# Performance work log

Hardware: AMD Instinct MI355X
Metric: run time of the kernel (lower is better)

Reference implementation:

```python
import jax, jax.numpy as jnp
import numpy as np

# static sizes
B, N_PER, D, H, L, DFF, IN_DIM = 32, 1024, 128, 4, 3, 2048, 64
N = B * N_PER
HD = D // H
EPS = 1e-5


def setup_inputs() -> dict:
    key = jax.random.key(0)
    ks = jax.random.split(key, 16)
    s = 0.02
    rn = lambda k, shp: jax.random.normal(k, shp, jnp.float32) * s
    return {
        "x": jax.random.normal(ks[0], (N, IN_DIM), jnp.float32),
        # uniform graph sizes -> static max_nodes; sorted graph ids
        "batch": jnp.repeat(jnp.arange(B, dtype=jnp.int32), N_PER),
        "W_in": rn(ks[1], (D, IN_DIM)),
        "b_in": rn(ks[2], (D,)),
        "Wqkv": rn(ks[3], (L, 3 * D, D)),
        "bqkv": rn(ks[4], (L, 3 * D)),
        "Wo": rn(ks[5], (L, D, D)),
        "bo": rn(ks[6], (L, D)),
        "W1": rn(ks[7], (L, DFF, D)),
        "b1": rn(ks[8], (L, DFF)),
        "W2": rn(ks[9], (L, D, DFF)),
        "b2": rn(ks[10], (L, D)),
        "ln1_g": jnp.ones((L, D), jnp.float32),
        "ln1_b": jnp.zeros((L, D), jnp.float32),
        "ln2_g": jnp.ones((L, D), jnp.float32),
        "ln2_b": jnp.zeros((L, D), jnp.float32),
    }


def _ln(x, g, b):
    m = x.mean(-1, keepdims=True)
    v = jnp.mean((x - m) ** 2, axis=-1, keepdims=True)
    return (x - m) / jnp.sqrt(v + EPS) * g + b


def _mha(h, Wqkv, bqkv, Wo, bo):
    # h: [B, S, D]
    qkv = h @ Wqkv.T + bqkv                      # [B, S, 3D]
    q, k, v = jnp.split(qkv, 3, axis=-1)
    q = q.reshape(B, -1, H, HD)
    k = k.reshape(B, -1, H, HD)
    v = v.reshape(B, -1, H, HD)
    att = jnp.einsum("bqhd,bkhd->bhqk", q, k) / np.sqrt(HD).astype(np.float32)
    p = jax.nn.softmax(att, axis=-1)
    o = jnp.einsum("bhqk,bkhd->bqhd", p, v).reshape(B, -1, D)
    return o @ Wo.T + bo


def reference(x, batch, W_in, b_in, Wqkv, bqkv, Wo, bo, W1, b1, W2, b2,
              ln1_g, ln1_b, ln2_g, ln2_b):
    # fused ragged -> padded: project all nodes once, scatter by (graph, pos)
    h = x @ W_in.T + b_in                        # [N, D]
    starts = jnp.searchsorted(batch, jnp.arange(B, dtype=batch.dtype))
    pos = jnp.arange(N, dtype=batch.dtype) - starts[batch]
    padded = jnp.zeros((B, N_PER, D), h.dtype).at[batch, pos].set(h)

    out = padded
    for l in range(L):  # post-LN TransformerEncoderLayer, dropout=eval
        a = _mha(out, Wqkv[l], bqkv[l], Wo[l], bo[l])
        out = _ln(out + a, ln1_g[l], ln1_b[l])
        f = jax.nn.relu(out @ W1[l].T + b1[l]) @ W2[l].T + b2[l]
        out = _ln(out + f, ln2_g[l], ln2_b[l])

    # mask derived from projected inputs, exactly as the original
    mask = (padded.sum(axis=2) != 0).astype(out.dtype)  # [B, S]
    return (out * mask[:, :, None]).sum(axis=1) / mask.sum(axis=1, keepdims=True)
```

## Files before the change

kernel.cpp:

```cpp
#include <hip/hip_runtime.h>
#include <hip/hip_bf16.h>
#include <stdint.h>

#define BB    32
#define NPER  1024
#define NTOT  32768
#define DD    128
#define HH    4
#define HD    32
#define LL    3
#define DFF   2048
#define INDIM 64
#define QKSCALE 0.17677669529663687f

typedef unsigned short u16;
typedef short bf16x8 __attribute__((ext_vector_type(8)));
typedef float f32x4 __attribute__((ext_vector_type(4)));

#define AS_GLOBAL(p) ((const __attribute__((address_space(1))) void*)(p))
#define AS_LDS(p)    ((__attribute__((address_space(3))) void*)(p))

__device__ __forceinline__ float bf2f(u16 v){
  unsigned u = ((unsigned)v) << 16; float f; __builtin_memcpy(&f, &u, 4); return f;
}
__device__ __forceinline__ u16 f2bf(float f){
  unsigned u; __builtin_memcpy(&u, &f, 4);
  unsigned lsb = (u >> 16) & 1u;
  u += 0x7fffu + lsb;
  return (u16)(u >> 16);
}

constexpr size_t OFF_FLAG   = 0;
constexpr size_t OFF_STARTS = 256;
constexpr size_t OFF_BIN    = 1024;
constexpr size_t OFF_BQKV   = OFF_BIN   + 128*4;
constexpr size_t OFF_BO     = OFF_BQKV  + 1152*4;
constexpr size_t OFF_B1     = OFF_BO    + 384*4;
constexpr size_t OFF_B2     = OFF_B1    + 6144*4;
constexpr size_t OFF_LN1G   = OFF_B2    + 384*4;
constexpr size_t OFF_LN1B   = OFF_LN1G  + 384*4;
constexpr size_t OFF_LN2G   = OFF_LN1B  + 384*4;
constexpr size_t OFF_LN2B   = OFF_LN2G  + 384*4;
constexpr size_t OFF_XB     = 40960;
constexpr size_t OFF_WINB   = OFF_XB    + (size_t)2097152*2;
constexpr size_t OFF_WQKVB  = OFF_WINB  + (size_t)8192*2;
constexpr size_t OFF_WOB    = OFF_WQKVB + (size_t)147456*2;
constexpr size_t OFF_W1B    = OFF_WOB   + (size_t)49152*2;
constexpr size_t OFF_W2B    = OFF_W1B   + (size_t)786432*2;
constexpr size_t OFF_CUR    = OFF_W2B   + (size_t)786432*2;
constexpr size_t OFF_TMP    = OFF_CUR   + (size_t)4194304*4;
constexpr size_t OFF_CURB   = OFF_TMP   + (size_t)4194304*4;
constexpr size_t OFF_QKVB   = OFF_CURB  + (size_t)4194304*2;
constexpr size_t OFF_ATTNOB = OFF_QKVB  + (size_t)12582912*2;
constexpr size_t OFF_ACTB   = OFF_ATTNOB+ (size_t)4194304*2;
constexpr size_t OFF_MASK   = OFF_ACTB  + (size_t)16777216*2;
constexpr size_t OFF_VT     = OFF_MASK  + (size_t)NTOT*4;
constexpr size_t OFF_RED    = OFF_VT    + (size_t)4096*1024*2;
constexpr size_t OFF_CNT    = OFF_RED   + (size_t)32*8*128*4;

__device__ __forceinline__ int plaus(unsigned bits){
  if ((bits << 1) == 0u) return 1;
  unsigned e = (bits >> 23) & 0xFFu;
  return (e >= 100u && e <= 140u) ? 1 : 0;
}
__global__ void detect_kernel(const unsigned* __restrict__ x, int* __restrict__ flag){
  __shared__ int red[256];
  int t = threadIdx.x, c = 0;
  for (int i = t; i < 2048; i += 256){
    unsigned w = x[i];
    c += (plaus(w << 16) & plaus(w & 0xFFFF0000u));
  }
  red[t] = c; __syncthreads();
  for (int s = 128; s > 0; s >>= 1){ if (t < s) red[t] += red[t+s]; __syncthreads(); }
  if (t == 0) *flag = (red[0] >= 1229) ? 1 : 0;
}

__global__ void starts_kernel(const int* __restrict__ batch, int* __restrict__ starts){
  int b = threadIdx.x;
  if (b < BB){
    int lo = 0, hi = NTOT;
    while (lo < hi){ int mid = (lo + hi) >> 1; if (batch[mid] < b) lo = mid + 1; else hi = mid; }
    starts[b] = lo;
  }
}

struct ConvSeg { const void* src; void* dst; int n; int tobf; };
struct ConvArgs { ConvSeg s[15]; };

__global__ __launch_bounds__(256) void convall_kernel(ConvArgs a, const int* __restrict__ flag){
  const int isb = *flag;
  const int blk = blockIdx.x;
  int seg = -1, base = 0, lb = 0;
  #pragma unroll
  for (int i = 0; i < 15; ++i){
    int nb = (a.s[i].n + 1023) >> 10;
    if (seg < 0){
      if (blk < base + nb){ seg = i; lb = blk - base; }
      base += nb;
    }
  }
  const ConvSeg sg = a.s[seg];
  const int idx = lb*1024 + threadIdx.x*4;
  if (idx >= sg.n) return;
  if (sg.tobf){
    u16* dst = (u16*)sg.dst + idx;
    if (isb){
      *(uint2*)dst = *(const uint2*)((const u16*)sg.src + idx);
    } else {
      const float* s4 = (const float*)sg.src + idx;
      dst[0] = f2bf(s4[0]); dst[1] = f2bf(s4[1]);
      dst[2] = f2bf(s4[2]); dst[3] = f2bf(s4[3]);
    }
  } else {
    float* dst = (float*)sg.dst + idx;
    if (isb){
      const u16* s4 = (const u16*)sg.src + idx;
      dst[0] = bf2f(s4[0]); dst[1] = bf2f(s4[1]);
      dst[2] = bf2f(s4[2]); dst[3] = bf2f(s4[3]);
    } else {
      *(float4*)dst = *(const float4*)((const float*)sg.src + idx);
    }
  }
}

__global__ __launch_bounds__(256) void gemm_bf16(
    const u16* __restrict__ A, int lda,
    const u16* __restrict__ W, int ldw,
    const float* __restrict__ bias,
    float* __restrict__ Cf, u16* __restrict__ Cb,
    int N, int K, int flags)
{
  __shared__ __align__(16) u16 At[64][32];
  __shared__ __align__(16) u16 Wt[64][32];
  const int t = threadIdx.x;
  const int m0 = blockIdx.x * 64, n0 = blockIdx.y * 64;
  const int wave = t >> 6, lane = t & 63;
  const int quad = lane >> 4, l16 = lane & 15;
  const int lr = t >> 2, lc = (t & 3) * 8;

  f32x4 acc[4];
  #pragma unroll
  for (int i = 0; i < 4; ++i){ acc[i][0]=0.f; acc[i][1]=0.f; acc[i][2]=0.f; acc[i][3]=0.f; }

  const u16* Arow = A + (size_t)(m0 + lr) * lda + lc;
  const u16* Wrow = W + (size_t)(n0 + lr) * ldw + lc;

  for (int k0 = 0; k0 < K; k0 += 32){
    uint4 av = *(const uint4*)(Arow + k0);
    uint4 wv = *(const uint4*)(Wrow + k0);
    __syncthreads();
    *(uint4*)&At[lr][lc] = av;
    *(uint4*)&Wt[lr][lc] = wv;
    __syncthreads();
    bf16x8 af = *(const bf16x8*)&At[wave*16 + l16][quad*8];
    #pragma unroll
    for (int nt = 0; nt < 4; ++nt){
      bf16x8 wf = *(const bf16x8*)&Wt[nt*16 + l16][quad*8];
      acc[nt] = __builtin_amdgcn_mfma_f32_16x16x32_bf16(af, wf, acc[nt], 0, 0, 0);
    }
  }
  const int row = m0 + wave*16 + quad*4;
  #pragma unroll
  for (int nt = 0; nt < 4; ++nt){
    const int col = n0 + nt*16 + l16;
    const float bv = bias ? bias[col] : 0.f;
    #pragma unroll
    for (int r = 0; r < 4; ++r){
      size_t idx = (size_t)(row + r) * N + col;
      float v = acc[nt][r] + bv;
      if (flags & 1) v = fmaxf(v, 0.f);
      if (Cf) Cf[idx] = v;
      if (Cb) Cb[idx] = f2bf(v);
    }
  }
}

__global__ __launch_bounds__(128) void scatter_kernel(
    const float* __restrict__ hlin, const int* __restrict__ batch,
    const int* __restrict__ starts, float* __restrict__ cur,
    u16* __restrict__ curb, float* __restrict__ mask)
{
  int i = blockIdx.x, t = threadIdx.x;
  int g = batch[i];
  int p = i - starts[g];
  float v = hlin[(size_t)i*DD + t];
  float s = v;
  #pragma unroll
  for (int off = 32; off; off >>= 1) s += __shfl_xor(s, off);
  __shared__ float sh[2];
  if ((t & 63) == 0) sh[t >> 6] = s;
  __syncthreads();
  float rowsum = sh[0] + sh[1];
  if ((unsigned)p < (unsigned)NPER && (unsigned)g < (unsigned)BB){
    size_t j = (size_t)g*NPER + p;
    cur[j*DD + t]  = v;
    curb[j*DD + t] = f2bf(v);
    if (t == 0) mask[j] = (rowsum != 0.f) ? 1.f : 0.f;
  }
}

__global__ __launch_bounds__(256) void fattn_kernel(
    const u16* __restrict__ qkvb,
    const u16* __restrict__ vt,
    u16* __restrict__ attnob)
{
  __shared__ __align__(16) u16 Klds[2][2048];
  __shared__ __align__(16) u16 Vl[2][2048];
  __shared__ __align__(16) u16 Pl[4][16*72];

  const int t = threadIdx.x;
  const int wave = t >> 6, lane = t & 63;
  const int quad = lane >> 4, l16 = lane & 15;
  const int q0 = blockIdx.x * 64;
  const int h = blockIdx.y, b = blockIdx.z;
  const size_t qkvbase = (size_t)b * NPER * 384;
  const u16* Kg = qkvb + qkvbase + 128 + h*HD;
  const u16* Vg = vt + (size_t)((b*HH + h)*HD) * NPER;

  bf16x8 qf;
  {
    const u16* qp = qkvb + qkvbase + (size_t)(q0 + wave*16 + l16)*384 + h*HD + quad*8;
    uint4 qv = *(const uint4*)qp;
    u16 raw[8]; __builtin_memcpy(raw, &qv, 16);
    #pragma unroll
    for (int j = 0; j < 8; ++j) qf[j] = (short)f2bf(bf2f(raw[j]) * QKSCALE);
  }

  const int vcv = wave*2 + (lane >> 5), vd = lane & 31;
  auto stage = [&](int buf, int kt){
    __builtin_amdgcn_global_load_lds(
        AS_GLOBAL(Kg + (size_t)(kt*64 + lane)*384 + wave*8),
        AS_LDS(&Klds[buf][wave*64*8]), 16, 0, 0);
    __builtin_amdgcn_global_load_lds(
        AS_GLOBAL(Vg + (size_t)vd*NPER + kt*64 + vcv*8),
        AS_LDS(&Vl[buf][wave*64*8]), 16, 0, 0);
  };

  float lsum = 0.f;
  f32x4 o0 = {0.f,0.f,0.f,0.f}, o1 = {0.f,0.f,0.f,0.f};
  u16* Pw = &Pl[wave][0];

  stage(0, 0);
  asm volatile("s_waitcnt vmcnt(0)" ::: "memory");
  __syncthreads();

  for (int kt = 0; kt < 16; ++kt){
    const int buf = kt & 1;
    if (kt + 1 < 16) stage(buf ^ 1, kt + 1);

    f32x4 sfr[4];
    #pragma unroll
    for (int nt = 0; nt < 4; ++nt){
      bf16x8 kf = *(const bf16x8*)&Klds[buf][(quad*64 + nt*16 + l16)*8];
      f32x4 z = {0.f,0.f,0.f,0.f};
      sfr[nt] = __builtin_amdgcn_mfma_f32_16x16x32_bf16(kf, qf, z, 0, 0, 0);
    }

    float ps = 0.f;
    #pragma unroll
    for (int nt = 0; nt < 4; ++nt){
      float e0 = __expf(sfr[nt][0]), e1 = __expf(sfr[nt][1]);
      float e2 = __expf(sfr[nt][2]), e3 = __expf(sfr[nt][3]);
      ps += (e0 + e1) + (e2 + e3);
      uint2 w;
      w.x = (unsigned)f2bf(e0) | ((unsigned)f2bf(e1) << 16);
      w.y = (unsigned)f2bf(e2) | ((unsigned)f2bf(e3) << 16);
      *(uint2*)&Pw[l16*72 + nt*16 + quad*4] = w;
    }
    ps += __shfl_xor(ps, 16);
    ps += __shfl_xor(ps, 32);
    lsum += ps;
    asm volatile("s_waitcnt lgkmcnt(0)" ::: "memory");

    #pragma unroll
    for (int kk = 0; kk < 2; ++kk){
      bf16x8 pf = *(const bf16x8*)&Pw[l16*72 + kk*32 + quad*8];
      bf16x8 v0 = *(const bf16x8*)&Vl[buf][((kk*4 + quad)*32 + l16)*8];
      bf16x8 v1 = *(const bf16x8*)&Vl[buf][((kk*4 + quad)*32 + 16 + l16)*8];
      o0 = __builtin_amdgcn_mfma_f32_16x16x32_bf16(pf, v0, o0, 0, 0, 0);
      o1 = __builtin_amdgcn_mfma_f32_16x16x32_bf16(pf, v1, o1, 0, 0, 0);
    }

    if (kt + 1 < 16){
      asm volatile("s_waitcnt vmcnt(0)" ::: "memory");
      __syncthreads();
    }
  }

  #pragma unroll
  for (int r = 0; r < 4; ++r){
    float inv = 1.f / __shfl(lsum, quad*4 + r);
    int row = q0 + wave*16 + quad*4 + r;
    size_t base = (size_t)(b*NPER + row)*DD + h*HD;
    attnob[base + l16]      = f2bf(o0[r] * inv);
    attnob[base + 16 + l16] = f2bf(o1[r] * inv);
  }
}

__device__ __forceinline__ void epilogue_ln64(
    const f32x4 O[8], int m0, int wave, int quad, int l16,
    const float* __restrict__ bias, const float* __restrict__ g,
    const float* __restrict__ beta, float* __restrict__ cur,
    u16* __restrict__ curb)
{
  #pragma unroll
  for (int rr = 0; rr < 4; ++rr){
    int row = m0 + wave*16 + quad*4 + rr;
    float vs[8], sum = 0.f;
    #pragma unroll
    for (int nt = 0; nt < 8; ++nt){
      int col = nt*16 + l16;
      float v = O[nt][rr] + bias[col] + cur[(size_t)row*DD + col];
      vs[nt] = v; sum += v;
    }
    sum += __shfl_xor(sum, 1); sum += __shfl_xor(sum, 2);
    sum += __shfl_xor(sum, 4); sum += __shfl_xor(sum, 8);
    float mean = sum * (1.f/DD);
    float sq = 0.f;
    #pragma unroll
    for (int nt = 0; nt < 8; ++nt){ float d = vs[nt] - mean; sq += d*d; }
    sq += __shfl_xor(sq, 1); sq += __shfl_xor(sq, 2);
    sq += __shfl_xor(sq, 4); sq += __shfl_xor(sq, 8);
    float rs = rsqrtf(sq * (1.f/DD) + 1e-5f);
    #pragma unroll
    for (int nt = 0; nt < 8; ++nt){
      int col = nt*16 + l16;
      float o = (vs[nt] - mean)*rs*g[col] + beta[col];
      cur[(size_t)row*DD + col]  = o;
      curb[(size_t)row*DD + col] = f2bf(o);
    }
  }
}

__global__ __launch_bounds__(256) void wgemm_kernel(
    const u16* __restrict__ A,
    const u16* __restrict__ Wbase,
    const float* __restrict__ biasb,
    int mode,
    u16* __restrict__ outb, int opitch,
    u16* __restrict__ vtout,
    float* __restrict__ cur, u16* __restrict__ curb,
    const float* __restrict__ g, const float* __restrict__ beta)
{
  __shared__ __align__(16) u16 Wl[16384];
  const int t = threadIdx.x, wave = t >> 6, lane = t & 63;
  const int quad = lane >> 4, l16 = lane & 15;
  const int m0 = blockIdx.x * 64, nb = blockIdx.y;
  const u16* Wsl = Wbase + (size_t)nb * 16384;
  const float* bias = biasb + nb * 128;

  #pragma unroll
  for (int j = 0; j < 8; ++j){
    int s = t + 256*j;
    int r = s >> 4, cx = (s & 15) ^ (r & 15);
    *(uint4*)&Wl[s*8] = *(const uint4*)(Wsl + (size_t)r*128 + cx*8);
  }
  bf16x8 af[4];
  #pragma unroll
  for (int kk = 0; kk < 4; ++kk)
    af[kk] = *(const bf16x8*)(A + (size_t)(m0 + wave*16 + l16)*128 + kk*32 + quad*8);
  __syncthreads();

  f32x4 O[8];
  #pragma unroll
  for (int nt = 0; nt < 8; ++nt){ O[nt][0]=0.f; O[nt][1]=0.f; O[nt][2]=0.f; O[nt][3]=0.f; }

  #pragma unroll
  for (int nt = 0; nt < 8; ++nt){
    int row = nt*16 + l16;
    bf16x8 wf[4];
    #pragma unroll
    for (int kk = 0; kk < 4; ++kk)
      wf[kk] = *(const bf16x8*)&Wl[(row*16 + ((kk*4 + quad) ^ l16))*8];
    #pragma unroll
    for (int kk = 0; kk < 4; ++kk)
      O[nt] = __builtin_amdgcn_mfma_f32_16x16x32_bf16(af[kk], wf[kk], O[nt], 0, 0, 0);
  }

  if (mode == 0){
    if (nb == 2 && vtout){
      int rowb = m0 + wave*16 + quad*4;
      int bg = rowb >> 10, s = rowb & 1023;
      #pragma unroll
      for (int nt = 0; nt < 8; ++nt){
        int col = nt*16 + l16;
        int hh = col >> 5, d = col & 31;
        float v0 = O[nt][0] + bias[col], v1 = O[nt][1] + bias[col];
        float v2 = O[nt][2] + bias[col], v3 = O[nt][3] + bias[col];
        uint2 w;
        w.x = (unsigned)f2bf(v0) | ((unsigned)f2bf(v1) << 16);
        w.y = (unsigned)f2bf(v2) | ((unsigned)f2bf(v3) << 16);
        *(uint2*)(vtout + (size_t)((bg*HH + hh)*HD + d)*NPER + s) = w;
      }
    } else {
      #pragma unroll
      for (int rr = 0; rr < 4; ++rr){
        int row = m0 + wave*16 + quad*4 + rr;
        #pragma unroll
        for (int nt = 0; nt < 8; ++nt){
          int col = nt*16 + l16;
          outb[(size_t)row*opitch + nb*128 + col] = f2bf(O[nt][rr] + bias[col]);
        }
      }
    }
  } else {
    epilogue_ln64(O, m0, wave, quad, l16, bias, g, beta, cur, curb);
  }
}

__global__ __launch_bounds__(256, 2) void ffn_kernel(
    const u16* __restrict__ Ag,
    const u16* __restrict__ W1g,
    const u16* __restrict__ W2g,
    const float* __restrict__ b1,
    const float* __restrict__ b2,
    const float* __restrict__ g, const float* __restrict__ beta,
    float* __restrict__ cur, u16* __restrict__ curb)
{
  __shared__ __align__(16) u16 W1l[2][8192];
  __shared__ __align__(16) u16 W2l[2][8192];
  __shared__ __align__(16) u16 Pl[4][16*72];

  const int t = threadIdx.x, wave = t >> 6, lane = t & 63;
  const int quad = lane >> 4, l16 = lane & 15;
  const int m0 = blockIdx.x * 64;
  u16* Pw = &Pl[wave][0];

  auto stage = [&](int buf, int dffc){
    #pragma unroll
    for (int i = 0; i < 4; ++i){
      const int s0 = wave*256 + i*64;
      const int s  = s0 + lane;
      { int r = s >> 4, cx = (s & 15) ^ (r & 15);
        __builtin_amdgcn_global_load_lds(
            AS_GLOBAL(W1g + (size_t)(dffc + r)*128 + cx*8),
            AS_LDS(&W1l[buf][s0*8]), 16, 0, 0); }
      { int r = s >> 3, cx = (s & 7) ^ (r & 7);
        __builtin_amdgcn_global_load_lds(
            AS_GLOBAL(W2g + (size_t)r*DFF + dffc + cx*8),
            AS_LDS(&W2l[buf][s0*8]), 16, 0, 0); }
    }
  };

  bf16x8 af[4];
  #pragma unroll
  for (int kk = 0; kk < 4; ++kk)
    af[kk] = *(const bf16x8*)(Ag + (size_t)(m0 + wave*16 + l16)*128 + kk*32 + quad*8);

  f32x4 O[8];
  #pragma unroll
  for (int nt = 0; nt < 8; ++nt){ O[nt][0]=0.f; O[nt][1]=0.f; O[nt][2]=0.f; O[nt][3]=0.f; }

  stage(0, 0);
  asm volatile("s_waitcnt vmcnt(0)" ::: "memory");
  __syncthreads();

  for (int c = 0; c < 32; ++c){
    const int buf = c & 1;
    if (c + 1 < 32) stage(buf ^ 1, (c + 1)*64);

    #pragma unroll
    for (int nt = 0; nt < 4; ++nt){
      int row = nt*16 + l16;
      bf16x8 wf[4];
      #pragma unroll
      for (int kk = 0; kk < 4; ++kk)
        wf[kk] = *(const bf16x8*)&W1l[buf][(row*16 + ((kk*4 + quad) ^ l16))*8];
      float b1v = b1[c*64 + row];
      f32x4 s = {0.f,0.f,0.f,0.f};
      #pragma unroll
      for (int kk = 0; kk < 4; ++kk)
        s = __builtin_amdgcn_mfma_f32_16x16x32_bf16(af[kk], wf[kk], s, 0, 0, 0);
      #pragma unroll
      for (int rr = 0; rr < 4; ++rr)
        Pw[(quad*4 + rr)*72 + nt*16 + l16] = f2bf(fmaxf(s[rr] + b1v, 0.f));
    }
    asm volatile("s_waitcnt lgkmcnt(0)" ::: "memory");

    bf16x8 pf[2];
    #pragma unroll
    for (int kk = 0; kk < 2; ++kk)
      pf[kk] = *(const bf16x8*)&Pw[l16*72 + kk*32 + quad*8];
    #pragma unroll
    for (int nt = 0; nt < 8; ++nt){
      int row = nt*16 + l16;
      bf16x8 wf[2];
      #pragma unroll
      for (int kk = 0; kk < 2; ++kk)
        wf[kk] = *(const bf16x8*)&W2l[buf][(row*8 + ((kk*4 + quad) ^ (l16 & 7)))*8];
      #pragma unroll
      for (int kk = 0; kk < 2; ++kk)
        O[nt] = __builtin_amdgcn_mfma_f32_16x16x32_bf16(pf[kk], wf[kk], O[nt], 0, 0, 0);
    }

    if (c + 1 < 32){
      asm volatile("s_waitcnt vmcnt(0)" ::: "memory");
      __syncthreads();
    }
  }

  epilogue_ln64(O, m0, wave, quad, l16, b2, g, beta, cur, curb);
}

__global__ __launch_bounds__(128) void reduce1_kernel(
    const float* __restrict__ cur, const float* __restrict__ mask,
    float* __restrict__ partial, float* __restrict__ cnt)
{
  int b = blockIdx.x, c = blockIdx.y, t = threadIdx.x;
  float acc = 0.f, cn = 0.f;
  for (int s = c*128; s < c*128 + 128; ++s){
    float mk = mask[b*NPER + s];
    acc += cur[(size_t)(b*NPER + s)*DD + t] * mk;
    cn += mk;
  }
  partial[(size_t)(b*8 + c)*DD + t] = acc;
  if (t == 0) cnt[b*8 + c] = cn;
}
__global__ __launch_bounds__(128) void reduce2_kernel(
    const float* __restrict__ partial, const float* __restrict__ cnt,
    const int* __restrict__ flag, void* __restrict__ out)
{
  int b = blockIdx.x, t = threadIdx.x;
  float acc = 0.f, cn = 0.f;
  #pragma unroll
  for (int c = 0; c < 8; ++c){
    acc += partial[(size_t)(b*8 + c)*DD + t];
    cn  += cnt[b*8 + c];
  }
  float val = acc / cn;
  if (*flag) ((u16*)out)[b*DD + t] = f2bf(val);
  else       ((float*)out)[b*DD + t] = val;
}

extern "C" void kernel_launch(void* const* d_in, const int* in_sizes, int n_in,
                              void* d_out, int out_size, void* d_ws, size_t ws_size,
                              hipStream_t stream)
{
  (void)in_sizes; (void)n_in; (void)out_size; (void)ws_size;
  char* ws = (char*)d_ws;
  int*   flag   = (int*)(ws + OFF_FLAG);
  int*   starts = (int*)(ws + OFF_STARTS);
  float* BIN  = (float*)(ws + OFF_BIN);
  float* BQKV = (float*)(ws + OFF_BQKV);
  float* BO   = (float*)(ws + OFF_BO);
  float* B1   = (float*)(ws + OFF_B1);
  float* B2   = (float*)(ws + OFF_B2);
  float* LN1G = (float*)(ws + OFF_LN1G);
  float* LN1B = (float*)(ws + OFF_LN1B);
  float* LN2G = (float*)(ws + OFF_LN2G);
  float* LN2B = (float*)(ws + OFF_LN2B);
  u16* XB    = (u16*)(ws + OFF_XB);
  u16* WINB  = (u16*)(ws + OFF_WINB);
  u16* WQKVB = (u16*)(ws + OFF_WQKVB);
  u16* WOB   = (u16*)(ws + OFF_WOB);
  u16* W1B   = (u16*)(ws + OFF_W1B);
  u16* W2B   = (u16*)(ws + OFF_W2B);
  float* CUR = (float*)(ws + OFF_CUR);
  float* TMP = (float*)(ws + OFF_TMP);
  u16* CURB  = (u16*)(ws + OFF_CURB);
  u16* QKVB  = (u16*)(ws + OFF_QKVB);
  u16* ATTNOB= (u16*)(ws + OFF_ATTNOB);
  float* MASK= (float*)(ws + OFF_MASK);
  u16* VT    = (u16*)(ws + OFF_VT);
  float* RED = (float*)(ws + OFF_RED);
  float* CNT = (float*)(ws + OFF_CNT);

  detect_kernel<<<1, 256, 0, stream>>>((const unsigned*)d_in[0], flag);
  starts_kernel<<<1, 64, 0, stream>>>((const int*)d_in[1], starts);

  ConvArgs ca;
  ca.s[0]  = { d_in[0],  XB,    NTOT*INDIM, 1 };
  ca.s[1]  = { d_in[2],  WINB,  DD*INDIM,   1 };
  ca.s[2]  = { d_in[4],  WQKVB, LL*3*DD*DD, 1 };
  ca.s[3]  = { d_in[6],  WOB,   LL*DD*DD,   1 };
  ca.s[4]  = { d_in[8],  W1B,   LL*DFF*DD,  1 };
  ca.s[5]  = { d_in[10], W2B,   LL*DD*DFF,  1 };
  ca.s[6]  = { d_in[3],  BIN,   DD,         0 };
  ca.s[7]  = { d_in[5],  BQKV,  LL*3*DD,    0 };
  ca.s[8]  = { d_in[7],  BO,    LL*DD,      0 };
  ca.s[9]  = { d_in[9],  B1,    LL*DFF,     0 };
  ca.s[10] = { d_in[11], B2,    LL*DD,      0 };
  ca.s[11] = { d_in[12], LN1G,  LL*DD,      0 };
  ca.s[12] = { d_in[13], LN1B,  LL*DD,      0 };
  ca.s[13] = { d_in[14], LN2G,  LL*DD,      0 };
  ca.s[14] = { d_in[15], LN2B,  LL*DD,      0 };
  int nblk = 0;
  for (int i = 0; i < 15; ++i) nblk += (ca.s[i].n + 1023) >> 10;
  convall_kernel<<<nblk, 256, 0, stream>>>(ca, flag);

  gemm_bf16<<<dim3(NTOT/64, DD/64), 256, 0, stream>>>(
      XB, INDIM, WINB, INDIM, BIN, TMP, nullptr, DD, INDIM, 0);
  scatter_kernel<<<NTOT, 128, 0, stream>>>(TMP, (const int*)d_in[1], starts, CUR, CURB, MASK);

  for (int l = 0; l < LL; ++l){
    wgemm_kernel<<<dim3(NTOT/64, 3), 256, 0, stream>>>(
        CURB, WQKVB + (size_t)l*3*DD*DD, BQKV + l*3*DD, 0,
        QKVB, 384, VT, nullptr, nullptr, nullptr, nullptr);
    fattn_kernel<<<dim3(NPER/64, HH, BB), 256, 0, stream>>>(QKVB, VT, ATTNOB);
    wgemm_kernel<<<dim3(NTOT/64, 1), 256, 0, stream>>>(
        ATTNOB, WOB + (size_t)l*DD*DD, BO + l*DD, 1,
        nullptr, 0, nullptr, CUR, CURB, LN1G + l*DD, LN1B + l*DD);
    ffn_kernel<<<dim3(NTOT/64), 256, 0, stream>>>(
        CURB, W1B + (size_t)l*DFF*DD, W2B + (size_t)l*DD*DFF,
        B1 + l*DFF, B2 + l*DD, LN2G + l*DD, LN2B + l*DD, CUR, CURB);
  }

  reduce1_kernel<<<dim3(BB, 8), 128, 0, stream>>>(CUR, MASK, RED, CNT);
  reduce2_kernel<<<BB, 128, 0, stream>>>(RED, CNT, flag, d_out);
}
```

Measured before the change: 508.7 us.

## Double FFN row tile to 128 so each wave reuses weight fragments

The fused FFN kernel now processes 128 rows per block, 32 rows per wave, so each W1/W2 tile staged in LDS and each fragment loaded into registers feeds two M-subtiles. This halves how often weights are streamed from global memory and LDS per output row. The GEMM1 MFMA operands are swapped so each lane produces four consecutive DFF columns, written as one 8-byte store into a new XOR-swizzled P scratch layout. The LN epilogue is inlined for the two subtiles. The cost is more accumulator registers, with launch bounds relaxed to 1 block per CU and half as many blocks in the grid.

```diff
diff --git a/kernel.cpp b/kernel.cpp
--- a/kernel.cpp
+++ b/kernel.cpp
@@ -408,7 +408,7 @@
   }
 }
 
-__global__ __launch_bounds__(256, 2) void ffn_kernel(
+__global__ __launch_bounds__(256, 1) void ffn_kernel(
     const u16* __restrict__ Ag,
     const u16* __restrict__ W1g,
     const u16* __restrict__ W2g,
@@ -419,11 +419,12 @@
 {
   __shared__ __align__(16) u16 W1l[2][8192];
   __shared__ __align__(16) u16 W2l[2][8192];
-  __shared__ __align__(16) u16 Pl[4][16*72];
+  __shared__ __align__(16) u16 Pl[4][2048];
 
   const int t = threadIdx.x, wave = t >> 6, lane = t & 63;
   const int quad = lane >> 4, l16 = lane & 15;
-  const int m0 = blockIdx.x * 64;
+  const int e = l16 & 7;
+  const int m0 = blockIdx.x * 128;
   u16* Pw = &Pl[wave][0];
 
   auto stage = [&](int buf, int dffc){
@@ -442,14 +443,18 @@
     }
   };
 
-  bf16x8 af[4];
-  #pragma unroll
-  for (int kk = 0; kk < 4; ++kk)
-    af[kk] = *(const bf16x8*)(Ag + (size_t)(m0 + wave*16 + l16)*128 + kk*32 + quad*8);
-
-  f32x4 O[8];
-  #pragma unroll
-  for (int nt = 0; nt < 8; ++nt){ O[nt][0]=0.f; O[nt][1]=0.f; O[nt][2]=0.f; O[nt][3]=0.f; }
+  bf16x8 af[2][4];
+  #pragma unroll
+  for (int mt = 0; mt < 2; ++mt)
+    #pragma unroll
+    for (int kk = 0; kk < 4; ++kk)
+      af[mt][kk] = *(const bf16x8*)(Ag + (size_t)(m0 + wave*32 + mt*16 + l16)*128 + kk*32 + quad*8);
+
+  f32x4 O[2][8];
+  #pragma unroll
+  for (int mt = 0; mt < 2; ++mt)
+    #pragma unroll
+    for (int nt = 0; nt < 8; ++nt){ O[mt][nt][0]=0.f; O[mt][nt][1]=0.f; O[mt][nt][2]=0.f; O[mt][nt][3]=0.f; }
 
   stage(0, 0);
   asm volatile("s_waitcnt vmcnt(0)" ::: "memory");
@@ -466,31 +471,41 @@
       #pragma unroll
       for (int kk = 0; kk < 4; ++kk)
         wf[kk] = *(const bf16x8*)&W1l[buf][(row*16 + ((kk*4 + quad) ^ l16))*8];
-      float b1v = b1[c*64 + row];
-      f32x4 s = {0.f,0.f,0.f,0.f};
-      #pragma unroll
-      for (int kk = 0; kk < 4; ++kk)
-        s = __builtin_amdgcn_mfma_f32_16x16x32_bf16(af[kk], wf[kk], s, 0, 0, 0);
-      #pragma unroll
-      for (int rr = 0; rr < 4; ++rr)
-        Pw[(quad*4 + rr)*72 + nt*16 + l16] = f2bf(fmaxf(s[rr] + b1v, 0.f));
+      f32x4 b1v = *(const f32x4*)&b1[c*64 + nt*16 + quad*4];
+      #pragma unroll
+      for (int mt = 0; mt < 2; ++mt){
+        f32x4 s = {0.f,0.f,0.f,0.f};
+        #pragma unroll
+        for (int kk = 0; kk < 4; ++kk)
+          s = __builtin_amdgcn_mfma_f32_16x16x32_bf16(wf[kk], af[mt][kk], s, 0, 0, 0);
+        float v0 = fmaxf(s[0] + b1v[0], 0.f), v1 = fmaxf(s[1] + b1v[1], 0.f);
+        float v2 = fmaxf(s[2] + b1v[2], 0.f), v3 = fmaxf(s[3] + b1v[3], 0.f);
+        uint2 w;
+        w.x = (unsigned)f2bf(v0) | ((unsigned)f2bf(v1) << 16);
+        w.y = (unsigned)f2bf(v2) | ((unsigned)f2bf(v3) << 16);
+        *(uint2*)&Pw[(mt*16 + l16)*64 + (((nt*2 + (quad >> 1)) ^ e) << 3) + ((quad & 1) << 2)] = w;
+      }
     }
     asm volatile("s_waitcnt lgkmcnt(0)" ::: "memory");
 
-    bf16x8 pf[2];
-    #pragma unroll
-    for (int kk = 0; kk < 2; ++kk)
-      pf[kk] = *(const bf16x8*)&Pw[l16*72 + kk*32 + quad*8];
+    bf16x8 pf[2][2];
+    #pragma unroll
+    for (int mt = 0; mt < 2; ++mt)
+      #pragma unroll
+      for (int kk = 0; kk < 2; ++kk)
+        pf[mt][kk] = *(const bf16x8*)&Pw[(mt*16 + l16)*64 + (((kk*4 + quad) ^ e) << 3)];
     #pragma unroll
     for (int nt = 0; nt < 8; ++nt){
       int row = nt*16 + l16;
       bf16x8 wf[2];
       #pragma unroll
       for (int kk = 0; kk < 2; ++kk)
-        wf[kk] = *(const bf16x8*)&W2l[buf][(row*8 + ((kk*4 + quad) ^ (l16 & 7)))*8];
-      #pragma unroll
-      for (int kk = 0; kk < 2; ++kk)
-        O[nt] = __builtin_amdgcn_mfma_f32_16x16x32_bf16(pf[kk], wf[kk], O[nt], 0, 0, 0);
+        wf[kk] = *(const bf16x8*)&W2l[buf][(row*8 + ((kk*4 + quad) ^ e))*8];
+      #pragma unroll
+      for (int mt = 0; mt < 2; ++mt)
+        #pragma unroll
+        for (int kk = 0; kk < 2; ++kk)
+          O[mt][nt] = __builtin_amdgcn_mfma_f32_16x16x32_bf16(pf[mt][kk], wf[kk], O[mt][nt], 0, 0, 0);
     }
 
     if (c + 1 < 32){
@@ -499,7 +514,36 @@
     }
   }
 
-  epilogue_ln64(O, m0, wave, quad, l16, b2, g, beta, cur, curb);
+  #pragma unroll
+  for (int mt = 0; mt < 2; ++mt){
+    #pragma unroll
+    for (int rr = 0; rr < 4; ++rr){
+      int row = m0 + wave*32 + mt*16 + quad*4 + rr;
+      float vs[8], sum = 0.f;
+      #pragma unroll
+      for (int nt = 0; nt < 8; ++nt){
+        int col = nt*16 + l16;
+        float v = O[mt][nt][rr] + b2[col] + cur[(size_t)row*DD + col];
+        vs[nt] = v; sum += v;
+      }
+      sum += __shfl_xor(sum, 1); sum += __shfl_xor(sum, 2);
+      sum += __shfl_xor(sum, 4); sum += __shfl_xor(sum, 8);
+      float mean = sum * (1.f/DD);
+      float sq = 0.f;
+      #pragma unroll
+      for (int nt = 0; nt < 8; ++nt){ float d = vs[nt] - mean; sq += d*d; }
+      sq += __shfl_xor(sq, 1); sq += __shfl_xor(sq, 2);
+      sq += __shfl_xor(sq, 4); sq += __shfl_xor(sq, 8);
+      float rs = rsqrtf(sq * (1.f/DD) + 1e-5f);
+      #pragma unroll
+      for (int nt = 0; nt < 8; ++nt){
+        int col = nt*16 + l16;
+        float o = (vs[nt] - mean)*rs*g[col] + beta[col];
+        cur[(size_t)row*DD + col]  = o;
+        curb[(size_t)row*DD + col] = f2bf(o);
+      }
+    }
+  }
 }
 
 __global__ __launch_bounds__(128) void reduce1_kernel(
@@ -600,7 +644,7 @@
     wgemm_kernel<<<dim3(NTOT/64, 1), 256, 0, stream>>>(
         ATTNOB, WOB + (size_t)l*DD*DD, BO + l*DD, 1,
         nullptr, 0, nullptr, CUR, CURB, LN1G + l*DD, LN1B + l*DD);
-    ffn_kernel<<<dim3(NTOT/64), 256, 0, stream>>>(
+    ffn_kernel<<<dim3(NTOT/128), 256, 0, stream>>>(
         CURB, W1B + (size_t)l*DFF*DD, W2B + (size_t)l*DD*DFF,
         B1 + l*DFF, B2 + l*DD, LN2G + l*DD, LN2B + l*DD, CUR, CURB);
   }
```

Result: slower. 607.9 us (+19.5%).

## Rewrite FFN kernel with 32x32x16 MFMA tiles and wave-pair work split

Applied to the files above, without the earlier changes.

The FFN kernel now uses 32x32x16 bf16 MFMA instructions instead of 16x16x32. Waves are organized as pairs, each pair owning 32 rows: each wave computes half of the hidden chunk and half of the output columns, and the pair shares the ReLU intermediate through LDS with a barrier. The intent is to raise MFMA efficiency and cut per-wave LDS weight reads, since each weight fragment now feeds a larger tile. The residual+LayerNorm epilogue is rewritten for the new accumulator layout, with cross-wave row reductions through shared memory. In exchange it adds an extra barrier per chunk and more register pressure from the 16-wide accumulators.

```diff
diff --git a/kernel.cpp b/kernel.cpp
--- a/kernel.cpp
+++ b/kernel.cpp
@@ -16,6 +16,7 @@
 typedef unsigned short u16;
 typedef short bf16x8 __attribute__((ext_vector_type(8)));
 typedef float f32x4 __attribute__((ext_vector_type(4)));
+typedef float f32x16 __attribute__((ext_vector_type(16)));
 
 #define AS_GLOBAL(p) ((const __attribute__((address_space(1))) void*)(p))
 #define AS_LDS(p)    ((__attribute__((address_space(3))) void*)(p))
@@ -419,12 +420,15 @@
 {
   __shared__ __align__(16) u16 W1l[2][8192];
   __shared__ __align__(16) u16 W2l[2][8192];
-  __shared__ __align__(16) u16 Pl[4][16*72];
+  __shared__ __align__(16) u16 Pl[2][32*72];
+  __shared__ float exs[2][2][32];
+  __shared__ float exq[2][2][32];
 
   const int t = threadIdx.x, wave = t >> 6, lane = t & 63;
-  const int quad = lane >> 4, l16 = lane & 15;
+  const int pair = wave >> 1, q = wave & 1;
+  const int a32 = lane & 31, h = lane >> 5;
   const int m0 = blockIdx.x * 64;
-  u16* Pw = &Pl[wave][0];
+  u16* Pp = &Pl[pair][0];
 
   auto stage = [&](int buf, int dffc){
     #pragma unroll
@@ -442,64 +446,130 @@
     }
   };
 
-  bf16x8 af[4];
-  #pragma unroll
-  for (int kk = 0; kk < 4; ++kk)
-    af[kk] = *(const bf16x8*)(Ag + (size_t)(m0 + wave*16 + l16)*128 + kk*32 + quad*8);
-
-  f32x4 O[8];
-  #pragma unroll
-  for (int nt = 0; nt < 8; ++nt){ O[nt][0]=0.f; O[nt][1]=0.f; O[nt][2]=0.f; O[nt][3]=0.f; }
+  bf16x8 af[8];
+  #pragma unroll
+  for (int kk = 0; kk < 8; ++kk)
+    af[kk] = *(const bf16x8*)(Ag + (size_t)(m0 + pair*32 + a32)*128 + kk*16 + h*8);
+
+  f32x16 O[2] = {{0.f}, {0.f}};
+  #pragma unroll
+  for (int nt = 0; nt < 2; ++nt)
+    #pragma unroll
+    for (int j = 0; j < 16; ++j) O[nt][j] = 0.f;
 
   stage(0, 0);
   asm volatile("s_waitcnt vmcnt(0)" ::: "memory");
   __syncthreads();
 
+  const int w1row = q*32 + a32;
   for (int c = 0; c < 32; ++c){
     const int buf = c & 1;
+    const int dffc = c*64;
     if (c + 1 < 32) stage(buf ^ 1, (c + 1)*64);
 
-    #pragma unroll
-    for (int nt = 0; nt < 4; ++nt){
-      int row = nt*16 + l16;
-      bf16x8 wf[4];
+    f32x16 s0, s1;
+    #pragma unroll
+    for (int j = 0; j < 16; ++j){ s0[j] = 0.f; s1[j] = 0.f; }
+    #pragma unroll
+    for (int kk = 0; kk < 8; kk += 2){
+      bf16x8 wfa = *(const bf16x8*)&W1l[buf][(w1row*16 + (((kk  )*2 + h) ^ (w1row & 15)))*8];
+      bf16x8 wfb = *(const bf16x8*)&W1l[buf][(w1row*16 + (((kk+1)*2 + h) ^ (w1row & 15)))*8];
+      s0 = __builtin_amdgcn_mfma_f32_32x32x16_bf16(wfa, af[kk],   s0, 0, 0, 0);
+      s1 = __builtin_amdgcn_mfma_f32_32x32x16_bf16(wfb, af[kk+1], s1, 0, 0, 0);
+    }
+    #pragma unroll
+    for (int gi = 0; gi < 4; ++gi){
+      int dffl = q*32 + gi*8 + h*4;
+      f32x4 b1v = *(const f32x4*)&b1[dffc + dffl];
+      float v0 = fmaxf(s0[gi*4+0] + s1[gi*4+0] + b1v[0], 0.f);
+      float v1 = fmaxf(s0[gi*4+1] + s1[gi*4+1] + b1v[1], 0.f);
+      float v2 = fmaxf(s0[gi*4+2] + s1[gi*4+2] + b1v[2], 0.f);
+      float v3 = fmaxf(s0[gi*4+3] + s1[gi*4+3] + b1v[3], 0.f);
+      uint2 w;
+      w.x = (unsigned)f2bf(v0) | ((unsigned)f2bf(v1) << 16);
+      w.y = (unsigned)f2bf(v2) | ((unsigned)f2bf(v3) << 16);
+      *(uint2*)&Pp[a32*72 + dffl] = w;
+    }
+    asm volatile("s_waitcnt lgkmcnt(0)\ns_barrier" ::: "memory");
+
+    bf16x8 pf[4];
+    #pragma unroll
+    for (int kk = 0; kk < 4; ++kk)
+      pf[kk] = *(const bf16x8*)&Pp[a32*72 + kk*16 + h*8];
+    #pragma unroll
+    for (int nt = 0; nt < 2; ++nt){
+      const int w2row = q*64 + nt*32 + a32;
+      f32x16 acc = O[nt];
       #pragma unroll
-      for (int kk = 0; kk < 4; ++kk)
-        wf[kk] = *(const bf16x8*)&W1l[buf][(row*16 + ((kk*4 + quad) ^ l16))*8];
-      float b1v = b1[c*64 + row];
-      f32x4 s = {0.f,0.f,0.f,0.f};
-      #pragma unroll
-      for (int kk = 0; kk < 4; ++kk)
-        s = __builtin_amdgcn_mfma_f32_16x16x32_bf16(af[kk], wf[kk], s, 0, 0, 0);
-      #pragma unroll
-      for (int rr = 0; rr < 4; ++rr)
-        Pw[(quad*4 + rr)*72 + nt*16 + l16] = f2bf(fmaxf(s[rr] + b1v, 0.f));
-    }
-    asm volatile("s_waitcnt lgkmcnt(0)" ::: "memory");
-
-    bf16x8 pf[2];
-    #pragma unroll
-    for (int kk = 0; kk < 2; ++kk)
-      pf[kk] = *(const bf16x8*)&Pw[l16*72 + kk*32 + quad*8];
-    #pragma unroll
-    for (int nt = 0; nt < 8; ++nt){
-      int row = nt*16 + l16;
-      bf16x8 wf[2];
-      #pragma unroll
-      for (int kk = 0; kk < 2; ++kk)
-        wf[kk] = *(const bf16x8*)&W2l[buf][(row*8 + ((kk*4 + quad) ^ (l16 & 7)))*8];
-      #pragma unroll
-      for (int kk = 0; kk < 2; ++kk)
-        O[nt] = __builtin_amdgcn_mfma_f32_16x16x32_bf16(pf[kk], wf[kk], O[nt], 0, 0, 0);
+      for (int kk = 0; kk < 4; ++kk){
+        bf16x8 wf = *(const bf16x8*)&W2l[buf][(w2row*8 + ((kk*2 + h) ^ (w2row & 7)))*8];
+        acc = __builtin_amdgcn_mfma_f32_32x32x16_bf16(pf[kk], wf, acc, 0, 0, 0);
+      }
+      O[nt] = acc;
     }
 
     if (c + 1 < 32){
-      asm volatile("s_waitcnt vmcnt(0)" ::: "memory");
-      __syncthreads();
-    }
-  }
-
-  epilogue_ln64(O, m0, wave, quad, l16, b2, g, beta, cur, curb);
+      asm volatile("s_waitcnt vmcnt(0) lgkmcnt(0)\ns_barrier" ::: "memory");
+    }
+  }
+
+  const int col0 = q*64 + a32, col1 = q*64 + 32 + a32;
+  const float g0 = g[col0], g1 = g[col1];
+  const float be0 = beta[col0], be1 = beta[col1];
+  const float bb0 = b2[col0], bb1 = b2[col1];
+
+  float vs0[16], vs1[16], srow[16];
+  #pragma unroll
+  for (int reg = 0; reg < 16; ++reg){
+    int rowl = (reg & 3) + 8*(reg >> 2) + 4*h;
+    size_t rb = (size_t)(m0 + pair*32 + rowl) * DD;
+    vs0[reg] = O[0][reg] + bb0 + cur[rb + col0];
+    vs1[reg] = O[1][reg] + bb1 + cur[rb + col1];
+    float s = vs0[reg] + vs1[reg];
+    s += __shfl_xor(s, 1); s += __shfl_xor(s, 2);
+    s += __shfl_xor(s, 4); s += __shfl_xor(s, 8); s += __shfl_xor(s, 16);
+    srow[reg] = s;
+  }
+  __syncthreads();
+  if (a32 == 0){
+    #pragma unroll
+    for (int reg = 0; reg < 16; ++reg)
+      exs[pair][q][(reg & 3) + 8*(reg >> 2) + 4*h] = srow[reg];
+  }
+  __syncthreads();
+  float mean[16];
+  #pragma unroll
+  for (int reg = 0; reg < 16; ++reg)
+    mean[reg] = (srow[reg] + exs[pair][q ^ 1][(reg & 3) + 8*(reg >> 2) + 4*h]) * (1.f/DD);
+
+  float qrow[16];
+  #pragma unroll
+  for (int reg = 0; reg < 16; ++reg){
+    float d0 = vs0[reg] - mean[reg], d1 = vs1[reg] - mean[reg];
+    float s = d0*d0 + d1*d1;
+    s += __shfl_xor(s, 1); s += __shfl_xor(s, 2);
+    s += __shfl_xor(s, 4); s += __shfl_xor(s, 8); s += __shfl_xor(s, 16);
+    qrow[reg] = s;
+  }
+  if (a32 == 0){
+    #pragma unroll
+    for (int reg = 0; reg < 16; ++reg)
+      exq[pair][q][(reg & 3) + 8*(reg >> 2) + 4*h] = qrow[reg];
+  }
+  __syncthreads();
+  #pragma unroll
+  for (int reg = 0; reg < 16; ++reg){
+    int rowl = (reg & 3) + 8*(reg >> 2) + 4*h;
+    float var = (qrow[reg] + exq[pair][q ^ 1][rowl]) * (1.f/DD);
+    float rs = rsqrtf(var + 1e-5f);
+    size_t rb = (size_t)(m0 + pair*32 + rowl) * DD;
+    float o0 = (vs0[reg] - mean[reg])*rs*g0 + be0;
+    float o1 = (vs1[reg] - mean[reg])*rs*g1 + be1;
+    cur[rb + col0]  = o0;
+    cur[rb + col1]  = o1;
+    curb[rb + col0] = f2bf(o0);
+    curb[rb + col1] = f2bf(o1);
+  }
 }
 
 __global__ __launch_bounds__(128) void reduce1_kernel(
```

Measured after the change: 526.3 us. +3.5%, slower.

## Restructure FFN kernel to 32x32 MFMA with register-shuffled hidden activations and split-K

Applied to the files above, without the earlier changes.

Rewrites the FFN kernel's inner loop to use 32x32x16 MFMA instead of 16x16x32. Waves are arranged as 2 row groups by 2 DFF halves, and the second GEMM is split over the DFF dimension across wave pairs. The intermediate ReLU activations now move between lane halves with cross-lane shuffles instead of a per-wave LDS round trip. A new epilogue reduces the two split-K partials through LDS scratch and then applies bias, residual and LayerNorm. This is meant to cut LDS traffic and MFMA instruction count per chunk, at the cost of more registers and an extra reduction step at the end.

```diff
diff --git a/kernel.cpp b/kernel.cpp
--- a/kernel.cpp
+++ b/kernel.cpp
@@ -16,6 +16,7 @@
 typedef unsigned short u16;
 typedef short bf16x8 __attribute__((ext_vector_type(8)));
 typedef float f32x4 __attribute__((ext_vector_type(4)));
+typedef float f32x16 __attribute__((ext_vector_type(16)));
 
 #define AS_GLOBAL(p) ((const __attribute__((address_space(1))) void*)(p))
 #define AS_LDS(p)    ((__attribute__((address_space(3))) void*)(p))
@@ -419,12 +420,11 @@
 {
   __shared__ __align__(16) u16 W1l[2][8192];
   __shared__ __align__(16) u16 W2l[2][8192];
-  __shared__ __align__(16) u16 Pl[4][16*72];
 
   const int t = threadIdx.x, wave = t >> 6, lane = t & 63;
-  const int quad = lane >> 4, l16 = lane & 15;
+  const int ag = wave >> 1, d = wave & 1;
+  const int a32 = lane & 31, h = lane >> 5;
   const int m0 = blockIdx.x * 64;
-  u16* Pw = &Pl[wave][0];
 
   auto stage = [&](int buf, int dffc){
     #pragma unroll
@@ -435,71 +435,122 @@
         __builtin_amdgcn_global_load_lds(
             AS_GLOBAL(W1g + (size_t)(dffc + r)*128 + cx*8),
             AS_LDS(&W1l[buf][s0*8]), 16, 0, 0); }
-      { int r = s >> 3, cx = (s & 7) ^ (r & 7);
+      { int col = s >> 3, c8 = (s & 7) ^ (col & 7);
         __builtin_amdgcn_global_load_lds(
-            AS_GLOBAL(W2g + (size_t)r*DFF + dffc + cx*8),
+            AS_GLOBAL(W2g + (size_t)col*DFF + dffc + c8*8),
             AS_LDS(&W2l[buf][s0*8]), 16, 0, 0); }
     }
   };
 
-  bf16x8 af[4];
-  #pragma unroll
-  for (int kk = 0; kk < 4; ++kk)
-    af[kk] = *(const bf16x8*)(Ag + (size_t)(m0 + wave*16 + l16)*128 + kk*32 + quad*8);
-
-  f32x4 O[8];
-  #pragma unroll
-  for (int nt = 0; nt < 8; ++nt){ O[nt][0]=0.f; O[nt][1]=0.f; O[nt][2]=0.f; O[nt][3]=0.f; }
+  bf16x8 af[8];
+  #pragma unroll
+  for (int kk = 0; kk < 8; ++kk)
+    af[kk] = *(const bf16x8*)(Ag + (size_t)(m0 + ag*32 + a32)*128 + kk*16 + h*8);
+
+  f32x16 O[4];
+  #pragma unroll
+  for (int nt = 0; nt < 4; ++nt)
+    #pragma unroll
+    for (int j = 0; j < 16; ++j) O[nt][j] = 0.f;
 
   stage(0, 0);
   asm volatile("s_waitcnt vmcnt(0)" ::: "memory");
   __syncthreads();
 
+  const int w1r = d*32 + a32;
   for (int c = 0; c < 32; ++c){
     const int buf = c & 1;
     if (c + 1 < 32) stage(buf ^ 1, (c + 1)*64);
 
-    #pragma unroll
-    for (int nt = 0; nt < 4; ++nt){
-      int row = nt*16 + l16;
-      bf16x8 wf[4];
+    f32x16 s0v, s1v;
+    #pragma unroll
+    for (int j = 0; j < 16; ++j){ s0v[j] = 0.f; s1v[j] = 0.f; }
+    #pragma unroll
+    for (int kk = 0; kk < 8; kk += 2){
+      bf16x8 wa = *(const bf16x8*)&W1l[buf][(w1r*16 + (((kk  )*2 + h) ^ (w1r & 15)))*8];
+      bf16x8 wb = *(const bf16x8*)&W1l[buf][(w1r*16 + (((kk+1)*2 + h) ^ (w1r & 15)))*8];
+      s0v = __builtin_amdgcn_mfma_f32_32x32x16_bf16(wa, af[kk],   s0v, 0, 0, 0);
+      s1v = __builtin_amdgcn_mfma_f32_32x32x16_bf16(wb, af[kk+1], s1v, 0, 0, 0);
+    }
+    unsigned pk[8];
+    #pragma unroll
+    for (int gi = 0; gi < 4; ++gi){
+      f32x4 bv = *(const f32x4*)&b1[c*64 + d*32 + gi*8 + 4*h];
+      float v0 = fmaxf(s0v[gi*4+0] + s1v[gi*4+0] + bv[0], 0.f);
+      float v1 = fmaxf(s0v[gi*4+1] + s1v[gi*4+1] + bv[1], 0.f);
+      float v2 = fmaxf(s0v[gi*4+2] + s1v[gi*4+2] + bv[2], 0.f);
+      float v3 = fmaxf(s0v[gi*4+3] + s1v[gi*4+3] + bv[3], 0.f);
+      pk[gi*2]   = (unsigned)f2bf(v0) | ((unsigned)f2bf(v1) << 16);
+      pk[gi*2+1] = (unsigned)f2bf(v2) | ((unsigned)f2bf(v3) << 16);
+    }
+
+    #pragma unroll
+    for (int kk = 0; kk < 2; ++kk){
+      const int gown = 2*kk + h, gsend = 2*kk + 1 - h;
+      unsigned own0 = pk[gown*2],  own1 = pk[gown*2 + 1];
+      unsigned rc0 = (unsigned)__shfl_xor((int)pk[gsend*2],     32);
+      unsigned rc1 = (unsigned)__shfl_xor((int)pk[gsend*2 + 1], 32);
+      union { unsigned u[4]; bf16x8 v; } fr;
+      fr.u[0] = h ? rc0  : own0;
+      fr.u[1] = h ? rc1  : own1;
+      fr.u[2] = h ? own0 : rc0;
+      fr.u[3] = h ? own1 : rc1;
       #pragma unroll
-      for (int kk = 0; kk < 4; ++kk)
-        wf[kk] = *(const bf16x8*)&W1l[buf][(row*16 + ((kk*4 + quad) ^ l16))*8];
-      float b1v = b1[c*64 + row];
-      f32x4 s = {0.f,0.f,0.f,0.f};
+      for (int nt = 0; nt < 4; ++nt){
+        int col = nt*32 + a32;
+        bf16x8 wf = *(const bf16x8*)&W2l[buf][(col*8 + ((d*4 + kk*2 + h) ^ (col & 7)))*8];
+        O[nt] = __builtin_amdgcn_mfma_f32_32x32x16_bf16(fr.v, wf, O[nt], 0, 0, 0);
+      }
+    }
+
+    if (c + 1 < 32){
+      asm volatile("s_waitcnt vmcnt(0) lgkmcnt(0)\ns_barrier" ::: "memory");
+    }
+  }
+
+  __syncthreads();
+  float* scratch = (float*)&W1l[0][0];
+  if (d == 1){
+    #pragma unroll
+    for (int reg = 0; reg < 16; ++reg){
+      int actl = (reg & 3) + 8*(reg >> 2) + 4*h;
       #pragma unroll
-      for (int kk = 0; kk < 4; ++kk)
-        s = __builtin_amdgcn_mfma_f32_16x16x32_bf16(af[kk], wf[kk], s, 0, 0, 0);
+      for (int nt = 0; nt < 4; ++nt)
+        scratch[ag*4096 + actl*128 + nt*32 + a32] = O[nt][reg];
+    }
+  }
+  __syncthreads();
+  if (d == 0){
+    #pragma unroll
+    for (int reg = 0; reg < 16; ++reg){
+      int actl = (reg & 3) + 8*(reg >> 2) + 4*h;
+      int row = m0 + ag*32 + actl;
+      float vs[4], sum = 0.f;
       #pragma unroll
-      for (int rr = 0; rr < 4; ++rr)
-        Pw[(quad*4 + rr)*72 + nt*16 + l16] = f2bf(fmaxf(s[rr] + b1v, 0.f));
-    }
-    asm volatile("s_waitcnt lgkmcnt(0)" ::: "memory");
-
-    bf16x8 pf[2];
-    #pragma unroll
-    for (int kk = 0; kk < 2; ++kk)
-      pf[kk] = *(const bf16x8*)&Pw[l16*72 + kk*32 + quad*8];
-    #pragma unroll
-    for (int nt = 0; nt < 8; ++nt){
-      int row = nt*16 + l16;
-      bf16x8 wf[2];
+      for (int nt = 0; nt < 4; ++nt){
+        int col = nt*32 + a32;
+        float v = O[nt][reg] + scratch[ag*4096 + actl*128 + col]
+                + b2[col] + cur[(size_t)row*DD + col];
+        vs[nt] = v; sum += v;
+      }
+      sum += __shfl_xor(sum, 1); sum += __shfl_xor(sum, 2);
+      sum += __shfl_xor(sum, 4); sum += __shfl_xor(sum, 8); sum += __shfl_xor(sum, 16);
+      float mean = sum * (1.f/DD);
+      float sq = 0.f;
       #pragma unroll
-      for (int kk = 0; kk < 2; ++kk)
-        wf[kk] = *(const bf16x8*)&W2l[buf][(row*8 + ((kk*4 + quad) ^ (l16 & 7)))*8];
+      for (int nt = 0; nt < 4; ++nt){ float dv = vs[nt] - mean; sq += dv*dv; }
+      sq += __shfl_xor(sq, 1); sq += __shfl_xor(sq, 2);
+      sq += __shfl_xor(sq, 4); sq += __shfl_xor(sq, 8); sq += __shfl_xor(sq, 16);
+      float rs = rsqrtf(sq * (1.f/DD) + 1e-5f);
       #pragma unroll
-      for (int kk = 0; kk < 2; ++kk)
-        O[nt] = __builtin_amdgcn_mfma_f32_16x16x32_bf16(pf[kk], wf[kk], O[nt], 0, 0, 0);
-    }
-
-    if (c + 1 < 32){
-      asm volatile("s_waitcnt vmcnt(0)" ::: "memory");
-      __syncthreads();
-    }
-  }
-
-  epilogue_ln64(O, m0, wave, quad, l16, b2, g, beta, cur, curb);
+      for (int nt = 0; nt < 4; ++nt){
+        int col = nt*32 + a32;
+        float o = (vs[nt] - mean)*rs*g[col] + beta[col];
+        cur[(size_t)row*DD + col]  = o;
+        curb[(size_t)row*DD + col] = f2bf(o);
+      }
+    }
+  }
 }
 
 __global__ __launch_bounds__(128) void reduce1_kernel(
```

After: 568.5 us. +11.8%, slower.
